# Optimization experiments

Measured on AMD Instinct MI355X. Metric: run time of the kernel, lower is better.

## Reference

```python
import jax, jax.numpy as jnp
import numpy as np
from jax import lax

K_NBR = 9  # K nearest neighbors
R = 2      # shuffle_scale


def pixel_unshuffle(x, r):
    B, C, H, W = x.shape
    x = x.reshape(B, C, H // r, r, W // r, r)
    return x.transpose(0, 1, 3, 5, 2, 4).reshape(B, C * r * r, H // r, W // r)


def pixel_shuffle(x, r):
    B, C, H, W = x.shape
    x = x.reshape(B, C // (r * r), r, r, H, W)
    return x.transpose(0, 1, 4, 2, 5, 3).reshape(B, C // (r * r), H * r, W * r)


def conv2d_same(x, w, b):
    y = lax.conv_general_dilated(x, w, (1, 1), 'SAME',
                                 dimension_numbers=('NCHW', 'OIHW', 'NCHW'))
    return y + b[None, :, None, None]


def convnn_branching_layer(x, idx, wa, ba, wb, bb, wp, bp):
    """Conv2d_ConvNN_Random_Branching with shuffle_pattern='BA'."""
    x = pixel_unshuffle(x, R)                      # (B, C*r^2, H/r, W/r)
    B, C, H, W = x.shape
    T = H * W
    # Branch 1: standard 3x3 conv
    y1 = conv2d_same(x, wa, ba)                    # (B, c1, H, W)
    # Branch 2: ConvNN on K nearest of N random samples
    xt = x.reshape(B, C, T)                        # tokens
    samp = xt[:, :, idx]                           # (B, C, N) random samples
    dots = jnp.einsum('bct,bcn->btn', xt, samp)
    xn = jnp.sum(xt * xt, axis=1)[:, :, None]      # (B, T, 1)
    sn = jnp.sum(samp * samp, axis=1)[:, None, :]  # (B, 1, N)
    dist = xn + sn - 2.0 * dots                    # squared euclidean (B, T, N)
    nbr = lax.top_k(-dist, K_NBR)[1]               # (B, T, K) indices into samples
    # gather neighbor features: (B, C, T*K)
    g = jnp.take_along_axis(samp, nbr.reshape(B, 1, T * K_NBR), axis=2)
    g = g.reshape(B, C, T, K_NBR)
    # Conv1d(kernel=K, stride=K) over stacked neighbors
    y2 = jnp.einsum('bctk,ock->bot', g, wb) + bb[None, :, None]
    y2 = y2.reshape(B, wb.shape[0], H, W)          # (B, c2, H, W)
    y = jax.nn.relu(jnp.concatenate([y1, y2], axis=1))
    y = conv2d_same(y, wp, bp)                     # 1x1 -> out*r^2 channels
    return pixel_shuffle(y, R)                     # (B, out, H*r, W*r)


def setup_inputs() -> dict:
    key = jax.random.key(0)
    ks = jax.random.split(key, 24)
    s = 0.02
    B = 256
    inp = {
        'x': jax.random.normal(ks[0], (B, 3, 32, 32), jnp.float32),
        'idx1': jax.random.randint(ks[1], (64,), 0, 256, jnp.int32),
        'idx2': jax.random.randint(ks[2], (64,), 0, 256, jnp.int32),
        # layer 1: Cin = 3*4 = 12, branches 16+16, out 16*4 = 64 pre-shuffle
        'w1a': jax.random.normal(ks[3], (16, 12, 3, 3), jnp.float32) * s,
        'b1a': jnp.zeros((16,), jnp.float32),
        'w1b': jax.random.normal(ks[4], (16, 12, 9), jnp.float32) * s,
        'b1b': jnp.zeros((16,), jnp.float32),
        'w1p': jax.random.normal(ks[5], (64, 32, 1, 1), jnp.float32) * s,
        'b1p': jnp.zeros((64,), jnp.float32),
        # layer 2: Cin = 16*4 = 64, branches 32+32, out 32*4 = 128 pre-shuffle
        'w2a': jax.random.normal(ks[6], (32, 64, 3, 3), jnp.float32) * s,
        'b2a': jnp.zeros((32,), jnp.float32),
        'w2b': jax.random.normal(ks[7], (32, 64, 9), jnp.float32) * s,
        'b2b': jnp.zeros((32,), jnp.float32),
        'w2p': jax.random.normal(ks[8], (128, 64, 1, 1), jnp.float32) * s,
        'b2p': jnp.zeros((128,), jnp.float32),
        # FC head
        'fc1w': jax.random.normal(ks[9], (1024, 32768), jnp.float32) * s,
        'fc1b': jnp.zeros((1024,), jnp.float32),
        'fc2w': jax.random.normal(ks[10], (10, 1024), jnp.float32) * s,
        'fc2b': jnp.zeros((10,), jnp.float32),
    }
    return inp


def reference(x, idx1, idx2, w1a, b1a, w1b, b1b, w1p, b1p,
              w2a, b2a, w2b, b2b, w2p, b2p, fc1w, fc1b, fc2w, fc2b):
    h = convnn_branching_layer(x, idx1, w1a, b1a, w1b, b1b, w1p, b1p)  # (B,16,32,32)
    h = convnn_branching_layer(h, idx2, w2a, b2a, w2b, b2b, w2p, b2p)  # (B,32,32,32)
    h = h.reshape(h.shape[0], -1)                   # (B, 32768)
    h = jax.nn.relu(h @ fc1w.T + fc1b)
    return h @ fc2w.T + fc2b                        # (B, num_classes)
```

## Files before the change

### kernel.cpp

```cpp
#include <hip/hip_runtime.h>
#include <cstdint>
#include <cstddef>


#define DI static __device__ __forceinline__

typedef __attribute__((ext_vector_type(8))) short short8;
typedef __attribute__((ext_vector_type(4))) float f32x4;

DI unsigned short f2bf(float v) {
  unsigned u = __builtin_bit_cast(unsigned, v);
  unsigned r = (u + 0x7FFFu + ((u >> 16) & 1u)) >> 16;
  return (unsigned short)r;
}
DI float bf2f(unsigned short h) {
  unsigned u = ((unsigned)h) << 16;
  return __builtin_bit_cast(float, u);
}

DI float xu1_at(const float* __restrict__ x, int b, int c, int t) {
  int h = t >> 4, w = t & 15;
  return x[(((size_t)b * 3 + (c >> 2)) * 32 + 2 * h + ((c >> 1) & 1)) * 32 + 2 * w + (c & 1)];
}

__global__ __launch_bounds__(256) void k_prepw(
    const float* __restrict__ w1b, float* __restrict__ wT1,
    const float* __restrict__ w2b, float* __restrict__ wT2,
    const float* __restrict__ w1p, float* __restrict__ wp1T,
    const float* __restrict__ w2p, float* __restrict__ wp2T,
    const float* __restrict__ w1a, float* __restrict__ wa1T,
    const float* __restrict__ w2a, float* __restrict__ wa2T)
{
  int i = blockIdx.x * 256 + threadIdx.x;
  if (i < 1728) {
    int k = i / 192, r = i % 192, c = r >> 4, o = r & 15;
    wT1[i] = w1b[((size_t)o * 12 + c) * 9 + k];
    return;
  }
  i -= 1728;
  if (i < 18432) {
    int k = i / 2048, r = i % 2048, c = r >> 5, o = r & 31;
    wT2[i] = w2b[((size_t)o * 64 + c) * 9 + k];
    return;
  }
  i -= 18432;
  if (i < 2048) { int ic = i >> 6, o = i & 63; wp1T[i] = w1p[(size_t)o * 32 + ic]; return; }
  i -= 2048;
  if (i < 8192) { int ic = i >> 7, o = i & 127; wp2T[i] = w2p[(size_t)o * 64 + ic]; return; }
  i -= 8192;
  if (i < 1728) {
    int o = i & 15, u = i >> 4, ic = u / 9, tp = u % 9;
    wa1T[i] = w1a[((size_t)o * 12 + ic) * 9 + tp];
    return;
  }
  i -= 1728;
  if (i < 18432) {
    int o = i & 31, u = i >> 5, ic = u / 9, tp = u % 9;
    wa2T[i] = w2a[((size_t)o * 64 + ic) * 9 + tp];
  }
}

template <int CIN, bool GATHER, int CCTOT, int OCT>
__global__ __launch_bounds__(256) void k_conv3x3(
    const float* __restrict__ xsrc, const float* __restrict__ xu,
    const float* __restrict__ waT, const float* __restrict__ bias,
    float* __restrict__ ycat)
{
  int b = blockIdx.x;
  int ocb = blockIdx.y * 16;
  __shared__ float xs[CIN * 256];
  int t = threadIdx.x;
  if (GATHER) {
    for (int i = t; i < CIN * 256; i += 256) {
      int c = i >> 8, tt = i & 255;
      xs[i] = xu1_at(xsrc, b, c, tt);
    }
  } else {
    for (int i = t; i < CIN * 256; i += 256) xs[i] = xu[(size_t)b * CIN * 256 + i];
  }
  __syncthreads();
  int tt = t & 127, og = t >> 7;
  int oc0 = ocb + og * 8;
  int h0 = tt >> 4, wc = tt & 15;
  float acc0[8], acc1[8];
#pragma unroll
  for (int o = 0; o < 8; ++o) { acc0[o] = bias[oc0 + o]; acc1[o] = acc0[o]; }
  bool vw0 = wc > 0, vw2 = wc < 15, vh0 = h0 > 0, vh7 = h0 < 7;
  bool m0v[9] = {vh0 && vw0, vh0, vh0 && vw2, vw0, true, vw2, vw0, true, vw2};
  bool m1v[9] = {vw0, true, vw2, vw0, true, vw2, vh7 && vw0, vh7, vh7 && vw2};
  int tc0[9], tc1[9];
#pragma unroll
  for (int dh = 0; dh < 3; ++dh)
#pragma unroll
    for (int dw = 0; dw < 3; ++dw) {
      int o0 = (h0 + dh - 1) * 16 + (wc + dw - 1);
      int o1 = (h0 + 8 + dh - 1) * 16 + (wc + dw - 1);
      tc0[dh * 3 + dw] = o0 < 0 ? 0 : (o0 > 255 ? 255 : o0);
      tc1[dh * 3 + dw] = o1 < 0 ? 0 : (o1 > 255 ? 255 : o1);
    }
#pragma unroll 2
  for (int ic = 0; ic < CIN; ++ic) {
    float xv0[9], xv1[9];
#pragma unroll
    for (int tp = 0; tp < 9; ++tp) {
      float v0 = xs[ic * 256 + tc0[tp]];
      float v1 = xs[ic * 256 + tc1[tp]];
      xv0[tp] = m0v[tp] ? v0 : 0.f;
      xv1[tp] = m1v[tp] ? v1 : 0.f;
    }
#pragma unroll
    for (int tp = 0; tp < 9; ++tp) {
      const float* wp = waT + ((size_t)ic * 9 + tp) * OCT + oc0;
      float4 wA = *(const float4*)wp;
      float4 wB = *(const float4*)(wp + 4);
      float wv[8] = {wA.x, wA.y, wA.z, wA.w, wB.x, wB.y, wB.z, wB.w};
#pragma unroll
      for (int o = 0; o < 8; ++o) {
        acc0[o] = fmaf(xv0[tp], wv[o], acc0[o]);
        acc1[o] = fmaf(xv1[tp], wv[o], acc1[o]);
      }
    }
  }
#pragma unroll
  for (int o = 0; o < 8; ++o) {
    ycat[((size_t)b * CCTOT + oc0 + o) * 256 + tt] = fmaxf(acc0[o], 0.f);
    ycat[((size_t)b * CCTOT + oc0 + o) * 256 + tt + 128] = fmaxf(acc1[o], 0.f);
  }
}

template <int C, int STR, bool GATHER>
__global__ __launch_bounds__(256) void k_prep(
    const float* __restrict__ xsrc, const float* __restrict__ xu,
    const int* __restrict__ idx,
    float* __restrict__ sampT, float* __restrict__ samp_cn,
    float* __restrict__ snvg)
{
  int b = blockIdx.x, t = threadIdx.x;
  __shared__ float sph[C * 64];
  __shared__ int idxs[64];
  if (t < 64) idxs[t] = idx[t];
  __syncthreads();
  for (int i = t; i < C * 64; i += 256) {
    int c = i >> 6, n = i & 63;
    int p = idxs[n];
    sph[i] = GATHER ? xu1_at(xsrc, b, c, p) : xu[((size_t)b * C + c) * 256 + p];
  }
  __syncthreads();
  for (int i = t; i < C * 64; i += 256) samp_cn[(size_t)b * C * 64 + i] = sph[i];
  for (int i = t; i < 64 * STR; i += 256) {
    int n = i / STR, c = i % STR;
    if (c < C) sampT[(size_t)b * 64 * STR + i] = sph[c * 64 + n];
  }
  if (t < 64) {
    float s;
    {
#pragma clang fp contract(off)
      s = 0.f;
      for (int c = 0; c < C; ++c) { float v = sph[c * 64 + t]; s += v * v; }
    }
    snvg[(size_t)b * 64 + t] = s;
  }
}

template <int C, int STR, bool GATHER>
__global__ __launch_bounds__(256) void k_nbr(
    const float* __restrict__ xsrc, const float* __restrict__ xu,
    const float* __restrict__ sampT, const float* __restrict__ snvg,
    int* __restrict__ nbr)
{
  int b = blockIdx.x, t = threadIdx.x;
  float xcol[C];
#pragma unroll
  for (int c = 0; c < C; ++c)
    xcol[c] = GATHER ? xu1_at(xsrc, b, c, t) : xu[((size_t)b * C + c) * 256 + t];
  float xn;
  {
#pragma clang fp contract(off)
    xn = 0.f;
#pragma unroll
    for (int c = 0; c < C; ++c) xn += xcol[c] * xcol[c];
  }
  float bd[9];
  int bn[9];
#pragma unroll
  for (int i = 0; i < 9; ++i) { bd[i] = __builtin_inff(); bn[i] = 1 << 30; }

#pragma unroll 1
  for (int n = 0; n < 64; ++n) {
    const float* sp = sampT + ((size_t)b * 64 + n) * STR;
    float snvn = snvg[(size_t)b * 64 + n];
    float d;
    {
#pragma clang fp contract(off)
      float dot = 0.f;
#pragma unroll
      for (int c = 0; c < C; ++c) dot = fmaf(xcol[c], sp[c], dot);
      d = (xn + snvn) - 2.f * dot;
    }
    if (d < bd[8] || (d == bd[8] && n < bn[8])) {
      float dc = d;
      int nc = n;
#pragma unroll
      for (int i = 0; i < 9; ++i) {
        bool sw = (dc < bd[i]) || (dc == bd[i] && nc < bn[i]);
        float ob = bd[i]; int on = bn[i];
        bd[i] = sw ? dc : ob; bn[i] = sw ? nc : on;
        dc = sw ? ob : dc;   nc = sw ? on : nc;
      }
    }
  }
#pragma unroll
  for (int k = 0; k < 9; ++k) nbr[((size_t)b * 9 + k) * 256 + t] = bn[k];
}

template <int C, int OPT, int OTOT, int CCTOT, int OCBASE>
__global__ __launch_bounds__(256) void k_einsum(
    const float* __restrict__ samp_cn,
    const int* __restrict__ nbr,
    const float* __restrict__ wT,
    const float* __restrict__ bb,
    float* __restrict__ ycat)
{
  int b = blockIdx.x, t = threadIdx.x;
  int tt = t & 127, og = t >> 7;
  int o0 = og * OPT;
  __shared__ float samps[C * 64];
  for (int i = t; i < C * 64; i += 256)
    samps[i] = samp_cn[(size_t)b * C * 64 + i];
  int bnA[9], bnB[9];
#pragma unroll
  for (int k = 0; k < 9; ++k) {
    bnA[k] = nbr[((size_t)b * 9 + k) * 256 + tt];
    bnB[k] = nbr[((size_t)b * 9 + k) * 256 + tt + 128];
  }
  __syncthreads();
  float acc0[OPT], acc1[OPT];
#pragma unroll
  for (int o = 0; o < OPT; ++o) { acc0[o] = bb[o0 + o]; acc1[o] = acc0[o]; }
#pragma unroll 1
  for (int k = 0; k < 9; ++k) {
    int n0 = bnA[k], n1 = bnB[k];
#pragma unroll 2
    for (int c = 0; c < C; ++c) {
      float sv0 = samps[c * 64 + n0];
      float sv1 = samps[c * 64 + n1];
      const float* wp = wT + ((size_t)k * C + c) * OTOT + o0;
#pragma unroll
      for (int oq = 0; oq < OPT / 4; ++oq) {
        float4 wv = ((const float4*)wp)[oq];
        float w4[4] = {wv.x, wv.y, wv.z, wv.w};
#pragma unroll
        for (int j = 0; j < 4; ++j) {
          acc0[oq * 4 + j] = fmaf(sv0, w4[j], acc0[oq * 4 + j]);
          acc1[oq * 4 + j] = fmaf(sv1, w4[j], acc1[oq * 4 + j]);
        }
      }
    }
  }
#pragma unroll
  for (int o = 0; o < OPT; ++o) {
    ycat[((size_t)b * CCTOT + OCBASE + o0 + o) * 256 + tt] = fmaxf(acc0[o], 0.f);
    ycat[((size_t)b * CCTOT + OCBASE + o0 + o) * 256 + tt + 128] = fmaxf(acc1[o], 0.f);
  }
}

template <int CIN, int OPT, int OCTOT, bool SHUF>
__global__ __launch_bounds__(256) void k_conv1x1(
    const float* __restrict__ yin, const float* __restrict__ wpT,
    const float* __restrict__ bias, float* __restrict__ out)
{
  int b = blockIdx.x, ocb = blockIdx.y * 2 * OPT, t = threadIdx.x;
  int tt = t & 127, og = t >> 7;
  int o0 = ocb + og * OPT;
  __shared__ float ys[CIN * 256];
  for (int i = t; i < CIN * 256; i += 256) ys[i] = yin[(size_t)b * CIN * 256 + i];
  __syncthreads();
  float acc0[OPT], acc1[OPT];
#pragma unroll
  for (int o = 0; o < OPT; ++o) { acc0[o] = bias[o0 + o]; acc1[o] = acc0[o]; }
#pragma unroll 2
  for (int ic = 0; ic < CIN; ++ic) {
    float sv0 = ys[ic * 256 + tt];
    float sv1 = ys[ic * 256 + tt + 128];
    const float* wp = wpT + (size_t)ic * OCTOT + o0;
#pragma unroll
    for (int oq = 0; oq < OPT / 4; ++oq) {
      float4 wv = ((const float4*)wp)[oq];
      float w4[4] = {wv.x, wv.y, wv.z, wv.w};
#pragma unroll
      for (int j = 0; j < 4; ++j) {
        acc0[oq * 4 + j] = fmaf(sv0, w4[j], acc0[oq * 4 + j]);
        acc1[oq * 4 + j] = fmaf(sv1, w4[j], acc1[oq * 4 + j]);
      }
    }
  }
  int h0 = tt >> 4, wc = tt & 15;
#pragma unroll
  for (int o = 0; o < OPT; ++o) {
    int ogl = o0 + o;
    if (SHUF) {
      int f0 = (ogl >> 2) * 1024 + (2 * h0 + ((ogl >> 1) & 1)) * 32 + (2 * wc + (ogl & 1));
      int f1 = (ogl >> 2) * 1024 + (2 * (h0 + 8) + ((ogl >> 1) & 1)) * 32 + (2 * wc + (ogl & 1));
      out[(size_t)b * 32768 + f0] = acc0[o];
      out[(size_t)b * 32768 + f1] = acc1[o];
    } else {
      out[((size_t)b * OCTOT + ogl) * 256 + tt] = acc0[o];
      out[((size_t)b * OCTOT + ogl) * 256 + tt + 128] = acc1[o];
    }
  }
}

__global__ __launch_bounds__(256, 2) void k_fc1(
    const float* __restrict__ A, const float* __restrict__ W,
    float* __restrict__ parts)
{
  constexpr int KTOT = 32768;
  constexpr int LDT = 40;
  __shared__ unsigned short Ah[128 * LDT], Am[128 * LDT], Al[128 * LDT];
  int t = threadIdx.x;
  int nb = blockIdx.x, mb = blockIdx.y, sb = blockIdx.z;
  int m0 = mb * 128, n0 = nb * 128, k0 = sb * 1024;
  int wave = t >> 6, lane = t & 63;
  int q = lane >> 4, m16 = lane & 15;

  f32x4 acc[8][2];
#pragma unroll
  for (int mt = 0; mt < 8; ++mt)
#pragma unroll
    for (int nt = 0; nt < 2; ++nt) acc[mt][nt] = (f32x4){0.f, 0.f, 0.f, 0.f};

  int arow = t >> 1, acol = (t & 1) * 16;
  const float* Ap = A + (size_t)(m0 + arow) * KTOT + k0 + acol;
  const float* W0 = W + (size_t)(n0 + wave * 32 + m16) * KTOT + k0 + q * 8;
  const float* W1 = W + (size_t)(n0 + wave * 32 + 16 + m16) * KTOT + k0 + q * 8;

  float4 aR0 = *(const float4*)(Ap + 0);
  float4 aR1 = *(const float4*)(Ap + 4);
  float4 aR2 = *(const float4*)(Ap + 8);
  float4 aR3 = *(const float4*)(Ap + 12);
  float4 w0a = *(const float4*)(W0), w0b = *(const float4*)(W0 + 4);
  float4 w1a = *(const float4*)(W1), w1b = *(const float4*)(W1 + 4);

  for (int ks = 0; ks < 1024; ks += 32) {
    int ksn = (ks + 32 < 1024) ? ks + 32 : 0;
    float4 nA0 = *(const float4*)(Ap + ksn);
    float4 nA1 = *(const float4*)(Ap + ksn + 4);
    float4 nA2 = *(const float4*)(Ap + ksn + 8);
    float4 nA3 = *(const float4*)(Ap + ksn + 12);
    float4 nW0a = *(const float4*)(W0 + ksn), nW0b = *(const float4*)(W0 + ksn + 4);
    float4 nW1a = *(const float4*)(W1 + ksn), nW1b = *(const float4*)(W1 + ksn + 4);

    short8 bh[2], bm[2], bl[2];
    {
      float wf0[8] = {w0a.x, w0a.y, w0a.z, w0a.w, w0b.x, w0b.y, w0b.z, w0b.w};
      float wf1[8] = {w1a.x, w1a.y, w1a.z, w1a.w, w1b.x, w1b.y, w1b.z, w1b.w};
#pragma unroll
      for (int j = 0; j < 8; ++j) {
        unsigned short h = f2bf(wf0[j]); float r1 = wf0[j] - bf2f(h);
        unsigned short m = f2bf(r1);
        bh[0][j] = (short)h; bm[0][j] = (short)m; bl[0][j] = (short)f2bf(r1 - bf2f(m));
        h = f2bf(wf1[j]); r1 = wf1[j] - bf2f(h);
        m = f2bf(r1);
        bh[1][j] = (short)h; bm[1][j] = (short)m; bl[1][j] = (short)f2bf(r1 - bf2f(m));
      }
    }
    short8 vh0, vh1, vm0, vm1, vl0, vl1;
    {
      float av[16] = {aR0.x, aR0.y, aR0.z, aR0.w, aR1.x, aR1.y, aR1.z, aR1.w,
                      aR2.x, aR2.y, aR2.z, aR2.w, aR3.x, aR3.y, aR3.z, aR3.w};
#pragma unroll
      for (int j = 0; j < 8; ++j) {
        {
          float v = av[j];
          unsigned short h = f2bf(v); float r1 = v - bf2f(h);
          unsigned short m = f2bf(r1);
          vh0[j] = (short)h; vm0[j] = (short)m; vl0[j] = (short)f2bf(r1 - bf2f(m));
        }
        {
          float v = av[j + 8];
          unsigned short h = f2bf(v); float r1 = v - bf2f(h);
          unsigned short m = f2bf(r1);
          vh1[j] = (short)h; vm1[j] = (short)m; vl1[j] = (short)f2bf(r1 - bf2f(m));
        }
      }
    }
    __syncthreads();
    {
      int off = arow * LDT + acol;
      *(short8*)&Ah[off] = vh0; *(short8*)&Ah[off + 8] = vh1;
      *(short8*)&Am[off] = vm0; *(short8*)&Am[off + 8] = vm1;
      *(short8*)&Al[off] = vl0; *(short8*)&Al[off + 8] = vl1;
    }
    __syncthreads();
#pragma unroll
    for (int mt = 0; mt < 8; ++mt) {
      int aoff = (mt * 16 + m16) * LDT + q * 8;
      short8 ah = *(const short8*)&Ah[aoff];
      short8 am = *(const short8*)&Am[aoff];
      short8 al = *(const short8*)&Al[aoff];
#pragma unroll
      for (int nt = 0; nt < 2; ++nt) {
        acc[mt][nt] = __builtin_amdgcn_mfma_f32_16x16x32_bf16(al, bh[nt], acc[mt][nt], 0, 0, 0);
        acc[mt][nt] = __builtin_amdgcn_mfma_f32_16x16x32_bf16(am, bm[nt], acc[mt][nt], 0, 0, 0);
        acc[mt][nt] = __builtin_amdgcn_mfma_f32_16x16x32_bf16(ah, bl[nt], acc[mt][nt], 0, 0, 0);
        acc[mt][nt] = __builtin_amdgcn_mfma_f32_16x16x32_bf16(am, bh[nt], acc[mt][nt], 0, 0, 0);
        acc[mt][nt] = __builtin_amdgcn_mfma_f32_16x16x32_bf16(ah, bm[nt], acc[mt][nt], 0, 0, 0);
        acc[mt][nt] = __builtin_amdgcn_mfma_f32_16x16x32_bf16(ah, bh[nt], acc[mt][nt], 0, 0, 0);
      }
    }
    aR0 = nA0; aR1 = nA1; aR2 = nA2; aR3 = nA3;
    w0a = nW0a; w0b = nW0b; w1a = nW1a; w1b = nW1b;
  }
  float* P = parts + (size_t)sb * 262144;
#pragma unroll
  for (int mt = 0; mt < 8; ++mt)
#pragma unroll
    for (int nt = 0; nt < 2; ++nt)
#pragma unroll
      for (int r2 = 0; r2 < 4; ++r2) {
        int m = m0 + mt * 16 + q * 4 + r2;
        int n = n0 + wave * 32 + nt * 16 + m16;
        P[(size_t)m * 1024 + n] = acc[mt][nt][r2];
      }
}

__global__ __launch_bounds__(256) void k_fc1_reduce(const float* __restrict__ parts,
                                                    const float* __restrict__ bias,
                                                    float* __restrict__ h1) {
  int i = blockIdx.x * 256 + threadIdx.x;
  float s = 0.f;
#pragma unroll
  for (int sb = 0; sb < 32; ++sb) s += parts[(size_t)sb * 262144 + i];
  h1[i] = fmaxf(s + bias[i & 1023], 0.f);
}

__global__ __launch_bounds__(256) void k_fc2(const float* __restrict__ h1,
                                             const float* __restrict__ w,
                                             const float* __restrict__ bias,
                                             float* __restrict__ out)
{
  int m = blockIdx.x, tid = threadIdx.x;
  __shared__ float hs[1024];
  __shared__ float ps[256];
  for (int i = tid; i < 1024; i += 256) hs[i] = h1[(size_t)m * 1024 + i];
  __syncthreads();
  int n = tid >> 4, sl = tid & 15;
  float p = 0.f;
  if (n < 10) {
    const float* wr = w + (size_t)n * 1024 + sl * 64;
    const float* hr = hs + sl * 64;
#pragma unroll 8
    for (int j = 0; j < 64; ++j) p = fmaf(hr[j], wr[j], p);
  }
  ps[tid] = p;
  __syncthreads();
  if (sl == 0 && n < 10) {
    float s = 0.f;
#pragma unroll
    for (int q = 0; q < 16; ++q) s += ps[n * 16 + q];
    out[(size_t)m * 10 + n] = s + bias[n];
  }
}

extern "C" void kernel_launch(void* const* d_in, const int* in_sizes, int n_in,
                              void* d_out, int out_size, void* d_ws, size_t ws_size,
                              hipStream_t stream) {
  (void)in_sizes; (void)n_in; (void)out_size; (void)ws_size;
  const float* x    = (const float*)d_in[0];
  const int*   idx1 = (const int*)d_in[1];
  const int*   idx2 = (const int*)d_in[2];
  const float* w1a  = (const float*)d_in[3];
  const float* b1a  = (const float*)d_in[4];
  const float* w1b  = (const float*)d_in[5];
  const float* b1b  = (const float*)d_in[6];
  const float* w1p  = (const float*)d_in[7];
  const float* b1p  = (const float*)d_in[8];
  const float* w2a  = (const float*)d_in[9];
  const float* b2a  = (const float*)d_in[10];
  const float* w2b  = (const float*)d_in[11];
  const float* b2b  = (const float*)d_in[12];
  const float* w2p  = (const float*)d_in[13];
  const float* b2p  = (const float*)d_in[14];
  const float* fc1w = (const float*)d_in[15];
  const float* fc1b = (const float*)d_in[16];
  const float* fc2w = (const float*)d_in[17];
  const float* fc2b = (const float*)d_in[18];

  float* ws    = (float*)d_ws;
  float* xu2   = ws + 0;
  float* ycat1 = ws + 4194304;
  float* ycat2 = ws + 4194304;
  float* WGT   = ws + 8388608;
  float* wT1   = WGT + 0;
  float* wT2   = WGT + 1728;
  float* wp1T  = WGT + 20160;
  float* wp2T  = WGT + 22208;
  float* wa1T  = WGT + 30400;
  float* wa2T  = WGT + 32128;
  float* h1    = ws + 8650752;
  float* hshuf = ws + 10485760;
  float* H        = ws + 10485760;
  int*   nbr      = (int*)(H + 0);
  float* sampT1   = H + 589824;
  float* snv1     = H + 851968;
  float* sampT2   = H + 868352;
  float* snv2     = H + 1916928;
  float* samp_cn1 = H + 1933312;
  float* samp_cn2 = H + 2129920;
  float* parts = ws + 0;
  float* out   = (float*)d_out;

  k_prepw<<<198, 256, 0, stream>>>(w1b, wT1, w2b, wT2, w1p, wp1T, w2p, wp2T, w1a, wa1T, w2a, wa2T);
  k_conv3x3<12, true, 32, 16><<<dim3(256, 1), 256, 0, stream>>>(x, nullptr, wa1T, b1a, ycat1);
  k_prep<12, 16, true><<<256, 256, 0, stream>>>(x, nullptr, idx1, sampT1, samp_cn1, snv1);
  k_nbr<12, 16, true><<<256, 256, 0, stream>>>(x, nullptr, sampT1, snv1, nbr);
  k_einsum<12, 8, 16, 32, 16><<<256, 256, 0, stream>>>(samp_cn1, nbr, wT1, b1b, ycat1);
  k_conv1x1<32, 32, 64, false><<<dim3(256, 1), 256, 0, stream>>>(ycat1, wp1T, b1p, xu2);
  k_conv3x3<64, false, 64, 32><<<dim3(256, 2), 256, 0, stream>>>(nullptr, xu2, wa2T, b2a, ycat2);
  k_prep<64, 64, false><<<256, 256, 0, stream>>>(nullptr, xu2, idx2, sampT2, samp_cn2, snv2);
  k_nbr<64, 64, false><<<256, 256, 0, stream>>>(nullptr, xu2, sampT2, snv2, nbr);
  k_einsum<64, 16, 32, 64, 32><<<256, 256, 0, stream>>>(samp_cn2, nbr, wT2, b2b, ycat2);
  k_conv1x1<64, 32, 128, true><<<dim3(256, 2), 256, 0, stream>>>(ycat2, wp2T, b2p, hshuf);
  k_fc1<<<dim3(8, 2, 32), 256, 0, stream>>>(hshuf, fc1w, parts);
  k_fc1_reduce<<<1024, 256, 0, stream>>>(parts, fc1b, h1);
  k_fc2<<<256, 256, 0, stream>>>(h1, fc2w, fc2b, out);
}
```

Measured before the change: 686.1 us.

## Double-buffer fc1 LDS tiles and use packed bf16 conversion for 3-way split

The fc1 GEMM kernel now keeps two LDS buffers for the A operand's bf16 hi/mid/lo splits. The next tile is converted and written while the current one feeds MFMA, so each iteration needs one barrier instead of two. The fp32-to-bf16x3 split now uses the hardware v_cvt_pk_bf16_f32 instruction on pairs instead of manual rounding bit tricks. The MFMA section is wrapped in s_setprio, and the LDS row stride shrinks from 40 to 36. The doubled LDS footprint and longer register lifetimes may hurt occupancy, and the narrower stride may change bank-conflict behaviour.

Result: slower. 796.8 us (+16.1%).

```diff
diff --git a/kernel.cpp b/kernel.cpp
--- a/kernel.cpp
+++ b/kernel.cpp
@@ -7,6 +7,7 @@
 
 typedef __attribute__((ext_vector_type(8))) short short8;
 typedef __attribute__((ext_vector_type(4))) float f32x4;
+typedef __attribute__((ext_vector_type(4))) unsigned u32x4;
 
 DI unsigned short f2bf(float v) {
   unsigned u = __builtin_bit_cast(unsigned, v);
@@ -16,6 +17,21 @@
 DI float bf2f(unsigned short h) {
   unsigned u = ((unsigned)h) << 16;
   return __builtin_bit_cast(float, u);
+}
+
+DI unsigned cvtpk_bf16(float lo, float hi) {
+  unsigned r;
+  asm("v_cvt_pk_bf16_f32 %0, %1, %2" : "=v"(r) : "v"(lo), "v"(hi));
+  return r;
+}
+DI void split_pair(float v0, float v1, unsigned& h, unsigned& m, unsigned& l) {
+  h = cvtpk_bf16(v0, v1);
+  float r0 = v0 - __builtin_bit_cast(float, h << 16);
+  float r1 = v1 - __builtin_bit_cast(float, h & 0xFFFF0000u);
+  m = cvtpk_bf16(r0, r1);
+  float s0 = r0 - __builtin_bit_cast(float, m << 16);
+  float s1 = r1 - __builtin_bit_cast(float, m & 0xFFFF0000u);
+  l = cvtpk_bf16(s0, s1);
 }
 
 DI float xu1_at(const float* __restrict__ x, int b, int c, int t) {
@@ -310,13 +326,36 @@
   }
 }
 
+constexpr int FC1_LDT = 36;
+
+DI void conv_writeA(unsigned short* AhB, unsigned short* AmB, unsigned short* AlB,
+                    int off, float4 a0, float4 a1, float4 a2, float4 a3) {
+  float av[16] = {a0.x, a0.y, a0.z, a0.w, a1.x, a1.y, a1.z, a1.w,
+                  a2.x, a2.y, a2.z, a2.w, a3.x, a3.y, a3.z, a3.w};
+  u32x4 H[2], M[2], L[2];
+#pragma unroll
+  for (int g = 0; g < 2; ++g)
+#pragma unroll
+    for (int p = 0; p < 4; ++p) {
+      unsigned h, m, l;
+      split_pair(av[g * 8 + 2 * p], av[g * 8 + 2 * p + 1], h, m, l);
+      H[g][p] = h; M[g][p] = m; L[g][p] = l;
+    }
+  *(short8*)&AhB[off] = __builtin_bit_cast(short8, H[0]);
+  *(short8*)&AhB[off + 8] = __builtin_bit_cast(short8, H[1]);
+  *(short8*)&AmB[off] = __builtin_bit_cast(short8, M[0]);
+  *(short8*)&AmB[off + 8] = __builtin_bit_cast(short8, M[1]);
+  *(short8*)&AlB[off] = __builtin_bit_cast(short8, L[0]);
+  *(short8*)&AlB[off + 8] = __builtin_bit_cast(short8, L[1]);
+}
+
 __global__ __launch_bounds__(256, 2) void k_fc1(
     const float* __restrict__ A, const float* __restrict__ W,
     float* __restrict__ parts)
 {
   constexpr int KTOT = 32768;
-  constexpr int LDT = 40;
-  __shared__ unsigned short Ah[128 * LDT], Am[128 * LDT], Al[128 * LDT];
+  constexpr int LDT = FC1_LDT;
+  __shared__ unsigned short Ah[2][128 * LDT], Am[2][128 * LDT], Al[2][128 * LDT];
   int t = threadIdx.x;
   int nb = blockIdx.x, mb = blockIdx.y, sb = blockIdx.z;
   int m0 = mb * 128, n0 = nb * 128, k0 = sb * 1024;
@@ -330,74 +369,66 @@
     for (int nt = 0; nt < 2; ++nt) acc[mt][nt] = (f32x4){0.f, 0.f, 0.f, 0.f};
 
   int arow = t >> 1, acol = (t & 1) * 16;
+  int aoffw = arow * LDT + acol;
   const float* Ap = A + (size_t)(m0 + arow) * KTOT + k0 + acol;
   const float* W0 = W + (size_t)(n0 + wave * 32 + m16) * KTOT + k0 + q * 8;
   const float* W1 = W + (size_t)(n0 + wave * 32 + 16 + m16) * KTOT + k0 + q * 8;
 
-  float4 aR0 = *(const float4*)(Ap + 0);
-  float4 aR1 = *(const float4*)(Ap + 4);
-  float4 aR2 = *(const float4*)(Ap + 8);
-  float4 aR3 = *(const float4*)(Ap + 12);
+  {
+    float4 p0 = *(const float4*)(Ap + 0);
+    float4 p1 = *(const float4*)(Ap + 4);
+    float4 p2 = *(const float4*)(Ap + 8);
+    float4 p3 = *(const float4*)(Ap + 12);
+    conv_writeA(Ah[0], Am[0], Al[0], aoffw, p0, p1, p2, p3);
+  }
+  float4 aR0 = *(const float4*)(Ap + 32);
+  float4 aR1 = *(const float4*)(Ap + 36);
+  float4 aR2 = *(const float4*)(Ap + 40);
+  float4 aR3 = *(const float4*)(Ap + 44);
   float4 w0a = *(const float4*)(W0), w0b = *(const float4*)(W0 + 4);
   float4 w1a = *(const float4*)(W1), w1b = *(const float4*)(W1 + 4);
-
-  for (int ks = 0; ks < 1024; ks += 32) {
-    int ksn = (ks + 32 < 1024) ? ks + 32 : 0;
-    float4 nA0 = *(const float4*)(Ap + ksn);
-    float4 nA1 = *(const float4*)(Ap + ksn + 4);
-    float4 nA2 = *(const float4*)(Ap + ksn + 8);
-    float4 nA3 = *(const float4*)(Ap + ksn + 12);
-    float4 nW0a = *(const float4*)(W0 + ksn), nW0b = *(const float4*)(W0 + ksn + 4);
-    float4 nW1a = *(const float4*)(W1 + ksn), nW1b = *(const float4*)(W1 + ksn + 4);
+  __syncthreads();
+
+  for (int i = 0; i < 32; ++i) {
+    int ks = i * 32;
+    int ka = (i + 2 < 32) ? ks + 64 : 0;
+    int kw = (i + 1 < 32) ? ks + 32 : 0;
+    float4 nA0 = *(const float4*)(Ap + ka);
+    float4 nA1 = *(const float4*)(Ap + ka + 4);
+    float4 nA2 = *(const float4*)(Ap + ka + 8);
+    float4 nA3 = *(const float4*)(Ap + ka + 12);
+    float4 nW0a = *(const float4*)(W0 + kw), nW0b = *(const float4*)(W0 + kw + 4);
+    float4 nW1a = *(const float4*)(W1 + kw), nW1b = *(const float4*)(W1 + kw + 4);
 
     short8 bh[2], bm[2], bl[2];
     {
       float wf0[8] = {w0a.x, w0a.y, w0a.z, w0a.w, w0b.x, w0b.y, w0b.z, w0b.w};
       float wf1[8] = {w1a.x, w1a.y, w1a.z, w1a.w, w1b.x, w1b.y, w1b.z, w1b.w};
-#pragma unroll
-      for (int j = 0; j < 8; ++j) {
-        unsigned short h = f2bf(wf0[j]); float r1 = wf0[j] - bf2f(h);
-        unsigned short m = f2bf(r1);
-        bh[0][j] = (short)h; bm[0][j] = (short)m; bl[0][j] = (short)f2bf(r1 - bf2f(m));
-        h = f2bf(wf1[j]); r1 = wf1[j] - bf2f(h);
-        m = f2bf(r1);
-        bh[1][j] = (short)h; bm[1][j] = (short)m; bl[1][j] = (short)f2bf(r1 - bf2f(m));
-      }
-    }
-    short8 vh0, vh1, vm0, vm1, vl0, vl1;
-    {
-      float av[16] = {aR0.x, aR0.y, aR0.z, aR0.w, aR1.x, aR1.y, aR1.z, aR1.w,
-                      aR2.x, aR2.y, aR2.z, aR2.w, aR3.x, aR3.y, aR3.z, aR3.w};
-#pragma unroll
-      for (int j = 0; j < 8; ++j) {
-        {
-          float v = av[j];
-          unsigned short h = f2bf(v); float r1 = v - bf2f(h);
-          unsigned short m = f2bf(r1);
-          vh0[j] = (short)h; vm0[j] = (short)m; vl0[j] = (short)f2bf(r1 - bf2f(m));
-        }
-        {
-          float v = av[j + 8];
-          unsigned short h = f2bf(v); float r1 = v - bf2f(h);
-          unsigned short m = f2bf(r1);
-          vh1[j] = (short)h; vm1[j] = (short)m; vl1[j] = (short)f2bf(r1 - bf2f(m));
-        }
-      }
-    }
-    __syncthreads();
-    {
-      int off = arow * LDT + acol;
-      *(short8*)&Ah[off] = vh0; *(short8*)&Ah[off + 8] = vh1;
-      *(short8*)&Am[off] = vm0; *(short8*)&Am[off + 8] = vm1;
-      *(short8*)&Al[off] = vl0; *(short8*)&Al[off + 8] = vl1;
-    }
-    __syncthreads();
+      u32x4 H0, M0, L0, H1, M1, L1;
+#pragma unroll
+      for (int p = 0; p < 4; ++p) {
+        unsigned h, m, l;
+        split_pair(wf0[2 * p], wf0[2 * p + 1], h, m, l);
+        H0[p] = h; M0[p] = m; L0[p] = l;
+        split_pair(wf1[2 * p], wf1[2 * p + 1], h, m, l);
+        H1[p] = h; M1[p] = m; L1[p] = l;
+      }
+      bh[0] = __builtin_bit_cast(short8, H0); bm[0] = __builtin_bit_cast(short8, M0);
+      bl[0] = __builtin_bit_cast(short8, L0);
+      bh[1] = __builtin_bit_cast(short8, H1); bm[1] = __builtin_bit_cast(short8, M1);
+      bl[1] = __builtin_bit_cast(short8, L1);
+    }
+
+    const unsigned short* AhR = Ah[i & 1];
+    const unsigned short* AmR = Am[i & 1];
+    const unsigned short* AlR = Al[i & 1];
+    __builtin_amdgcn_s_setprio(1);
 #pragma unroll
     for (int mt = 0; mt < 8; ++mt) {
       int aoff = (mt * 16 + m16) * LDT + q * 8;
-      short8 ah = *(const short8*)&Ah[aoff];
-      short8 am = *(const short8*)&Am[aoff];
-      short8 al = *(const short8*)&Al[aoff];
+      short8 ah = *(const short8*)&AhR[aoff];
+      short8 am = *(const short8*)&AmR[aoff];
+      short8 al = *(const short8*)&AlR[aoff];
 #pragma unroll
       for (int nt = 0; nt < 2; ++nt) {
         acc[mt][nt] = __builtin_amdgcn_mfma_f32_16x16x32_bf16(al, bh[nt], acc[mt][nt], 0, 0, 0);
@@ -408,6 +439,11 @@
         acc[mt][nt] = __builtin_amdgcn_mfma_f32_16x16x32_bf16(ah, bh[nt], acc[mt][nt], 0, 0, 0);
       }
     }
+    __builtin_amdgcn_s_setprio(0);
+
+    conv_writeA(Ah[(i + 1) & 1], Am[(i + 1) & 1], Al[(i + 1) & 1], aoffw,
+                aR0, aR1, aR2, aR3);
+    __syncthreads();
     aR0 = nA0; aR1 = nA1; aR2 = nA2; aR3 = nA3;
     w0a = nW0a; w0b = nW0b; w1a = nW1a; w1b = nW1b;
   }
```
